# Optimization experiments

Hardware: AMD Instinct MI355X
Metric: run time of the kernel (lower is better)

## Reference

```python
import jax, jax.numpy as jnp
import numpy as np
from jax import lax

T, B = 512, 512
IN_DIM, AUX_DIM, OUT_DIM = 4, 28, 32
G = IN_DIM + AUX_DIM + OUT_DIM  # gate_inputs = 64


def setup_inputs() -> dict:
    key = jax.random.key(0)
    ks = jax.random.split(key, 12)
    s = 0.05
    inp = {
        "xm": jax.random.uniform(ks[0], (T, B, IN_DIM), dtype=jnp.float32),
        "xa": jax.random.normal(ks[1], (T, B, AUX_DIM), dtype=jnp.float32),
        # in_gate (normalized sigmoid): Linear(G -> IN_DIM*OUT_DIM)
        "W_i": jax.random.normal(ks[2], (IN_DIM * OUT_DIM, G), dtype=jnp.float32) * s,
        "b_i": jnp.zeros((IN_DIM * OUT_DIM,), jnp.float32),
        # redistribution (normalized relu): Linear(G -> OUT_DIM*OUT_DIM)
        "W_r": jax.random.normal(ks[3], (OUT_DIM * OUT_DIM, G), dtype=jnp.float32) * s,
        "b_r": jnp.zeros((OUT_DIM * OUT_DIM,), jnp.float32),
        # out_gate: Linear(G -> OUT_DIM), bias init -3.0
        "W_o": jax.random.normal(ks[4], (OUT_DIM, G), dtype=jnp.float32) * s,
        "b_o": jnp.full((OUT_DIM,), -3.0, jnp.float32),
        # MR gate params: weight_s_yvm / weight_r_yvm are (out_features, in_features) = (OUT_DIM, G)
        "W_s": jax.random.normal(ks[5], (OUT_DIM, G), dtype=jnp.float32) * s,
        "W_rm": jax.random.normal(ks[6], (OUT_DIM, G), dtype=jnp.float32) * s,
        "b0": jnp.zeros((OUT_DIM,), jnp.float32),
        "ln_g": jnp.ones((OUT_DIM,), jnp.float32),
        "ln_b": jnp.zeros((OUT_DIM,), jnp.float32),
    }
    return inp


def _l1_normalize(a):
    # torch F.normalize(p=1, dim=-1)
    return a / jnp.maximum(jnp.sum(jnp.abs(a), axis=-1, keepdims=True), 1e-12)


def _layer_norm(x, g, b, eps=1e-5):
    mu = jnp.mean(x, axis=-1, keepdims=True)
    var = jnp.mean((x - mu) ** 2, axis=-1, keepdims=True)
    return (x - mu) * lax.rsqrt(var + eps) * g + b


def reference(xm, xa, W_i, b_i, W_r, b_r, W_o, b_o, W_s, W_rm, b0, ln_g, ln_b):
    Bn = xm.shape[1]
    exp_Ws = jnp.exp(W_s)            # [OUT_DIM, G]
    sig_Wr = jax.nn.sigmoid(W_rm.T)  # [G, OUT_DIM]

    def step(c, ins):
        xm_t, xa_t = ins  # [B, IN_DIM], [B, AUX_DIM]
        # c.norm(1) in torch is the scalar L1 norm over the whole matrix
        c_norm = c / (jnp.sum(jnp.abs(c)) + 1e-5)
        feat = jnp.concatenate([xm_t, xa_t, c_norm], axis=-1)  # [B, G]
        i = _l1_normalize(jax.nn.sigmoid(feat @ W_i.T + b_i).reshape(Bn, IN_DIM, OUT_DIM))
        r = _l1_normalize(jax.nn.relu(feat @ W_r.T + b_r).reshape(Bn, OUT_DIM, OUT_DIM))
        o = jax.nn.sigmoid(feat @ W_o.T + b_o)  # [B, OUT_DIM]
        m_new = jnp.einsum('bi,bio->bo', xm_t, i) + jnp.einsum('bo,bop->bp', c, r)
        # MR gate with f = 1 - o
        f = 1.0 - o
        ov0 = (c_norm - b0) @ exp_Ws          # [B, G]
        ov1 = _layer_norm(jnp.tanh(ov0) @ sig_Wr, ln_g, ln_b)  # [B, OUT_DIM]
        ov2 = ov1 - jax.nn.relu(ov1 - f)
        MR = jax.nn.relu(ov2 + 1.0 - f) + f - 1.0
        o_prime = o + MR
        h = o * m_new
        c_new = (1.0 - o_prime) * m_new
        MR_flow = MR * m_new
        return c_new, (h, c_new, o, MR, o_prime, MR_flow, h)

    c0 = jnp.zeros((Bn, OUT_DIM), xm.dtype)
    _, outs = lax.scan(step, c0, (xm, xa))
    # (hs, cs, os, mrs, o_prime_s, mr_flow_s, o_flow_s), each [T, B, OUT_DIM]
    return outs
```

## Files before the change

### kernel.cpp

```cpp
#include <hip/hip_runtime.h>


#define T_STEPS 512
#define OUTSZ 8388608ull

using bf16v8 = __attribute__((ext_vector_type(8))) short;
using f32v4  = __attribute__((ext_vector_type(4))) float;

__device__ __forceinline__ short f2b(float f) {
  union { float f; unsigned u; } x; x.f = f;
  unsigned r = x.u + 0x7fffu + ((x.u >> 16) & 1u);
  return (short)(r >> 16);
}
__device__ __forceinline__ float rcpf(float x) { return __builtin_amdgcn_rcpf(x); }

__device__ __forceinline__ float rowsum16(float v) {
  int t;
  float a = v;
  t = __builtin_amdgcn_mov_dpp(__builtin_bit_cast(int, a), 0x128, 0xF, 0xF, true);
  a += __builtin_bit_cast(float, t);
  t = __builtin_amdgcn_mov_dpp(__builtin_bit_cast(int, a), 0x124, 0xF, 0xF, true);
  a += __builtin_bit_cast(float, t);
  t = __builtin_amdgcn_mov_dpp(__builtin_bit_cast(int, a), 0x122, 0xF, 0xF, true);
  a += __builtin_bit_cast(float, t);
  t = __builtin_amdgcn_mov_dpp(__builtin_bit_cast(int, a), 0x121, 0xF, 0xF, true);
  a += __builtin_bit_cast(float, t);
  return a;
}

__global__ __launch_bounds__(512, 1) void mclstm_persistent(
    const float* __restrict__ g_xm, const float* __restrict__ g_xa,
    const float* __restrict__ g_Wi, const float* __restrict__ g_bi,
    const float* __restrict__ g_Wr, const float* __restrict__ g_br,
    const float* __restrict__ g_Wo, const float* __restrict__ g_bo,
    const float* __restrict__ g_Ws, const float* __restrict__ g_Wrm,
    const float* __restrict__ g_b0, const float* __restrict__ g_lng,
    const float* __restrict__ g_lnb,
    float* __restrict__ out, float* __restrict__ slots) {

  __shared__ __align__(16) float featx[2][16 * 36];
  __shared__ __align__(16) float cstate[16 * 36];
  __shared__ __align__(16) float gibuf[16 * 132];
  __shared__ __align__(16) float obuf[16 * 36];
  __shared__ __align__(16) float mpart[8][16 * 36];
  __shared__ __align__(16) float isump[128];
  __shared__ __align__(16) unsigned short tanhb[16 * 72];
  __shared__ __align__(16) unsigned short swzSig[4 * 512];
  __shared__ float s_bvec[64], s_lng[32], s_lnb[32];

  const int tid  = threadIdx.x;
  const int blk  = blockIdx.x;
  const int w    = tid >> 6;
  const int lane = tid & 63;
  const int q    = lane >> 4;
  const int m    = lane & 15;
  const f32v4 z4 = {0.f, 0.f, 0.f, 0.f};

  bf16v8 wr0[8], wr1[8];
  float brv[8];
#pragma unroll
  for (int t = 0; t < 8; ++t) {
    const int n = w * 128 + t * 16 + m;
    brv[t] = g_br[n];
#pragma unroll
    for (int kh = 0; kh < 2; ++kh) {
      const float* gp = g_Wr + n * 64 + kh * 32 + q * 8;
      f32v4 u0 = *(const f32v4*)gp;
      f32v4 u1 = *(const f32v4*)(gp + 4);
      bf16v8 fr;
#pragma unroll
      for (int j = 0; j < 4; ++j) { fr[j] = f2b(u0[j]); fr[4 + j] = f2b(u1[j]); }
      if (kh == 0) wr0[t] = fr; else wr1[t] = fr;
    }
  }
  bf16v8 wi0, wi1;
  const float gb = g_bi[w * 16 + m];
  {
    const int n = w * 16 + m;
#pragma unroll
    for (int kh = 0; kh < 2; ++kh) {
      const float* gp = g_Wi + n * 64 + kh * 32 + q * 8;
      f32v4 u0 = *(const f32v4*)gp;
      f32v4 u1 = *(const f32v4*)(gp + 4);
      bf16v8 fr;
#pragma unroll
      for (int j = 0; j < 4; ++j) { fr[j] = f2b(u0[j]); fr[4 + j] = f2b(u1[j]); }
      if (kh == 0) wi0 = fr; else wi1 = fr;
    }
  }
  bf16v8 bo0 = {0,0,0,0,0,0,0,0}, bo1 = bo0, be = bo0;
  float bov = 0.f;
  if (w < 2) {
    const int n = w * 16 + m;
    bov = g_bo[n];
#pragma unroll
    for (int kh = 0; kh < 2; ++kh) {
      bf16v8 fr, fs;
#pragma unroll
      for (int j = 0; j < 8; ++j) {
        fr[j] = f2b(g_Wo[n * 64 + kh * 32 + q * 8 + j]);
        float v = g_Wrm[n * 64 + kh * 32 + q * 8 + j];
        fs[j] = f2b(rcpf(1.0f + __expf(-v)));
      }
      if (kh == 0) bo0 = fr; else bo1 = fr;
      *(bf16v8*)&swzSig[(w * 2 + kh) * 512 + lane * 8] = fs;
    }
  }
  if (w >= 4) {
    const int n = (w - 4) * 16 + m;
    bf16v8 fr;
#pragma unroll
    for (int j = 0; j < 8; ++j) fr[j] = f2b(__expf(g_Ws[(q * 8 + j) * 64 + n]));
    be = fr;
  }
  if (tid < 64) {
    float a = 0.f;
    for (int o = 0; o < 32; ++o) a += g_b0[o] * __expf(g_Ws[o * 64 + tid]);
    s_bvec[tid] = a;
  }
  if (tid < 32) { s_lng[tid] = g_lng[tid]; s_lnb[tid] = g_lnb[tid]; }
  for (int i = tid; i < 16 * 36; i += 512) cstate[i] = 0.0f;
  {
    const int b2 = tid >> 5, k2 = tid & 31, rg = blk * 16 + b2;
    featx[0][b2 * 36 + k2] =
        (k2 < 4) ? g_xm[rg * 4 + k2] : g_xa[rg * 28 + k2 - 4];
  }
  __syncthreads();
  float bvl = (w >= 4) ? s_bvec[(w - 4) * 16 + m] : 0.f;

  float ph_h = 0, ph_cn = 0, ph_o = 0, ph_MR = 0, ph_op = 0, ph_mrf = 0;
  size_t ph_base = 0;

  for (int s = 0; s < T_STEPS; ++s) {
    if (s > 0) {
      out[ph_base] = ph_h;
      out[OUTSZ + ph_base] = ph_cn;
      out[2 * OUTSZ + ph_base] = ph_o;
      out[3 * OUTSZ + ph_base] = ph_MR;
      out[4 * OUTSZ + ph_base] = ph_op;
      out[5 * OUTSZ + ph_base] = ph_mrf;
      out[6 * OUTSZ + ph_base] = ph_h;
    }
    const int b2 = tid >> 5, k2 = tid & 31;
    const int sp = (s + 1 < T_STEPS) ? s + 1 : T_STEPS - 1;
    const float xv = (k2 < 4)
        ? g_xm[(size_t)sp * 2048 + (blk * 16 + b2) * 4 + k2]
        : g_xa[(size_t)sp * 14336 + (blk * 16 + b2) * 28 + k2 - 4];

    const float* fx = featx[s & 1];
    f32v4 x0 = *(const f32v4*)&fx[m * 36 + q * 8];
    f32v4 x1 = *(const f32v4*)&fx[m * 36 + q * 8 + 4];
    f32v4 c0 = *(const f32v4*)&cstate[m * 36 + q * 8];
    f32v4 c1 = *(const f32v4*)&cstate[m * 36 + q * 8 + 4];
    bf16v8 a0, a1;
#pragma unroll
    for (int j = 0; j < 4; ++j) {
      a0[j] = f2b(x0[j]); a0[4 + j] = f2b(x1[j]);
      a1[j] = f2b(c0[j]); a1[4 + j] = f2b(c1[j]);
    }

    f32v4 rx[8], rc[8];
#pragma unroll
    for (int t = 0; t < 8; ++t) {
      f32v4 cb = {brv[t], brv[t], brv[t], brv[t]};
      rx[t] = __builtin_amdgcn_mfma_f32_16x16x32_bf16(a0, wr0[t], cb, 0, 0, 0);
      rc[t] = __builtin_amdgcn_mfma_f32_16x16x32_bf16(a1, wr1[t], z4, 0, 0, 0);
    }
    f32v4 gxb = {gb, gb, gb, gb};
    f32v4 gxv = __builtin_amdgcn_mfma_f32_16x16x32_bf16(a0, wi0, gxb, 0, 0, 0);
    f32v4 gcv = __builtin_amdgcn_mfma_f32_16x16x32_bf16(a1, wi1, z4, 0, 0, 0);
    f32v4 oxv = z4, ocv = z4, ev = z4;
    if (w < 2) {
      f32v4 ob = {bov, bov, bov, bov};
      oxv = __builtin_amdgcn_mfma_f32_16x16x32_bf16(a0, bo0, ob, 0, 0, 0);
      ocv = __builtin_amdgcn_mfma_f32_16x16x32_bf16(a1, bo1, z4, 0, 0, 0);
    }
    if (w >= 4) {
      ev = __builtin_amdgcn_mfma_f32_16x16x32_bf16(a1, be, z4, 0, 0, 0);
    }
    f32v4 c4[4];
#pragma unroll
    for (int r = 0; r < 4; ++r)
      c4[r] = *(const f32v4*)&cstate[(q * 4 + r) * 36 + w * 4];
    featx[(s + 1) & 1][b2 * 36 + k2] = xv;

    float inv_;
    if (s > 0) {
      const float e = ((s >> 1) & 1) ? -1.0f : 1.0f;
      float* sl = slots + (s & 1) * 256 + lane * 4;
      float v0 = 0, v1 = 0, v2 = 0, v3 = 0;
      for (int it = 0; it < (1 << 18); ++it) {
        v0 = __hip_atomic_load(sl + 0, __ATOMIC_RELAXED, __HIP_MEMORY_SCOPE_AGENT);
        v1 = __hip_atomic_load(sl + 1, __ATOMIC_RELAXED, __HIP_MEMORY_SCOPE_AGENT);
        v2 = __hip_atomic_load(sl + 2, __ATOMIC_RELAXED, __HIP_MEMORY_SCOPE_AGENT);
        v3 = __hip_atomic_load(sl + 3, __ATOMIC_RELAXED, __HIP_MEMORY_SCOPE_AGENT);
        if (__all((v0 * e > 0.5f) && (v1 * e > 0.5f) &&
                  (v2 * e > 0.5f) && (v3 * e > 0.5f))) break;
        __builtin_amdgcn_s_sleep(1);
      }
      float sv = rowsum16((v0 + v1 + v2 + v3) * e - 4.0f);
      sv += __shfl_xor(sv, 16);
      sv += __shfl_xor(sv, 32);
      inv_ = rcpf(sv + 1e-5f);
    } else {
      inv_ = rcpf(1e-5f);
    }

    if (w >= 4) {
#pragma unroll
      for (int r = 0; r < 4; ++r) {
        float t0 = ev[r] * inv_ - bvl;
        float ex = __expf(2.0f * t0);
        float th = 1.0f - 2.0f * rcpf(ex + 1.0f);
        tanhb[(q * 4 + r) * 72 + (w - 4) * 16 + m] = (unsigned short)f2b(th);
      }
    }
    if (w < 2) {
#pragma unroll
      for (int r = 0; r < 4; ++r) {
        float t0 = oxv[r] + ocv[r] * inv_;
        obuf[(q * 4 + r) * 36 + w * 16 + m] = rcpf(1.0f + __expf(-t0));
      }
    }
    {
      float sg0, sg1, sg2, sg3;
      {
        float t0 = gxv[0] + gcv[0] * inv_; sg0 = rcpf(1.0f + __expf(-t0));
        t0 = gxv[1] + gcv[1] * inv_; sg1 = rcpf(1.0f + __expf(-t0));
        t0 = gxv[2] + gcv[2] * inv_; sg2 = rcpf(1.0f + __expf(-t0));
        t0 = gxv[3] + gcv[3] * inv_; sg3 = rcpf(1.0f + __expf(-t0));
      }
      gibuf[(q * 4 + 0) * 132 + w * 16 + m] = sg0;
      gibuf[(q * 4 + 1) * 132 + w * 16 + m] = sg1;
      gibuf[(q * 4 + 2) * 132 + w * 16 + m] = sg2;
      gibuf[(q * 4 + 3) * 132 + w * 16 + m] = sg3;
      sg0 = rowsum16(sg0); sg1 = rowsum16(sg1);
      sg2 = rowsum16(sg2); sg3 = rowsum16(sg3);
      if (m == 0) {
        f32v4 sv4 = {sg0, sg1, sg2, sg3};
        *(f32v4*)&isump[w * 16 + q * 4] = sv4;
      }
    }
    {
      f32v4 rr[8];
#pragma unroll
      for (int t = 0; t < 8; ++t)
#pragma unroll
        for (int r = 0; r < 4; ++r)
          rr[t][r] = fmaxf(fmaf(rc[t][r], inv_, rx[t][r]), 0.0f);
      float p0[4] = {0, 0, 0, 0}, p1[4] = {0, 0, 0, 0};
#pragma unroll
      for (int ol = 0; ol < 4; ++ol) {
        float s0 = rowsum16(rr[2 * ol][0] + rr[2 * ol + 1][0]);
        float s1 = rowsum16(rr[2 * ol][1] + rr[2 * ol + 1][1]);
        float s2 = rowsum16(rr[2 * ol][2] + rr[2 * ol + 1][2]);
        float s3 = rowsum16(rr[2 * ol][3] + rr[2 * ol + 1][3]);
        float cr0 = c4[0][ol] * rcpf(fmaxf(s0, 1e-12f));
        float cr1 = c4[1][ol] * rcpf(fmaxf(s1, 1e-12f));
        float cr2 = c4[2][ol] * rcpf(fmaxf(s2, 1e-12f));
        float cr3 = c4[3][ol] * rcpf(fmaxf(s3, 1e-12f));
        p0[0] += rr[2 * ol][0] * cr0; p1[0] += rr[2 * ol + 1][0] * cr0;
        p0[1] += rr[2 * ol][1] * cr1; p1[1] += rr[2 * ol + 1][1] * cr1;
        p0[2] += rr[2 * ol][2] * cr2; p1[2] += rr[2 * ol + 1][2] * cr2;
        p0[3] += rr[2 * ol][3] * cr3; p1[3] += rr[2 * ol + 1][3] * cr3;
      }
#pragma unroll
      for (int r = 0; r < 4; ++r) {
        mpart[w][(q * 4 + r) * 36 + m] = p0[r];
        mpart[w][(q * 4 + r) * 36 + 16 + m] = p1[r];
      }
    }
    __syncthreads();

    {
      bf16v8 a30 = *(const bf16v8*)&tanhb[m * 72 + q * 8];
      bf16v8 a31 = *(const bf16v8*)&tanhb[m * 72 + 32 + q * 8];
      bf16v8 b00 = *(const bf16v8*)&swzSig[0 * 512 + lane * 8];
      bf16v8 b01 = *(const bf16v8*)&swzSig[1 * 512 + lane * 8];
      bf16v8 b10 = *(const bf16v8*)&swzSig[2 * 512 + lane * 8];
      bf16v8 b11 = *(const bf16v8*)&swzSig[3 * 512 + lane * 8];
      f32v4 vA = __builtin_amdgcn_mfma_f32_16x16x32_bf16(a30, b00, z4, 0, 0, 0);
      vA = __builtin_amdgcn_mfma_f32_16x16x32_bf16(a31, b01, vA, 0, 0, 0);
      f32v4 vB = __builtin_amdgcn_mfma_f32_16x16x32_bf16(a30, b10, z4, 0, 0, 0);
      vB = __builtin_amdgcn_mfma_f32_16x16x32_bf16(a31, b11, vB, 0, 0, 0);
      const int b = tid >> 5, p = tid & 31;
      const int srcl = ((b >> 2) << 4) | (p & 15);
      float x00, x01, x10, x11;
      if ((w & 1) == 0) {
        x00 = __shfl(vA[0], srcl); x01 = __shfl(vB[0], srcl);
        x10 = __shfl(vA[1], srcl); x11 = __shfl(vB[1], srcl);
      } else {
        x00 = __shfl(vA[2], srcl); x01 = __shfl(vB[2], srcl);
        x10 = __shfl(vA[3], srcl); x11 = __shfl(vB[3], srcl);
      }
      const bool hiReg = (lane >> 5) != 0;
      const bool hiCol = (p >> 4) != 0;
      float vh0 = hiReg ? x10 : x00;
      float vh1 = hiReg ? x11 : x01;
      float x = hiCol ? vh1 : vh0;

      float s1v = rowsum16(x);      s1v += __shfl_xor(s1v, 16);
      float s2v = rowsum16(x * x);  s2v += __shfl_xor(s2v, 16);
      float mu = s1v * 0.03125f;
      float var = s2v * 0.03125f - mu * mu;
      float ln = (x - mu) * __builtin_amdgcn_rsqf(fmaxf(var, 0.0f) + 1e-5f) *
                     s_lng[p] + s_lnb[p];
      float o = obuf[b * 36 + p];
      float f = 1.0f - o;
      float MR = fmaxf(fminf(ln, f), f - 1.0f);
      float mn = 0.0f;
#pragma unroll
      for (int w2 = 0; w2 < 8; ++w2) mn += mpart[w2][b * 36 + p];
#pragma unroll
      for (int ii = 0; ii < 4; ++ii) {
        float rsi = rcpf(fmaxf(isump[(2 * ii) * 16 + b] +
                               isump[(2 * ii + 1) * 16 + b], 1e-12f));
        mn += fx[b * 36 + ii] * gibuf[b * 132 + ii * 32 + p] * rsi;
      }
      float op = o + MR;
      ph_h = o * mn;
      ph_cn = (1.0f - op) * mn;
      ph_o = o; ph_MR = MR; ph_op = op;
      ph_mrf = MR * mn;
      ph_base = (size_t)s * 16384 + (size_t)(blk * 16 + b) * 32 + p;
      cstate[b * 36 + p] = ph_cn;
      float aw = rowsum16(fabsf(ph_cn));
      aw += __shfl_xor(aw, 16);
      aw += __shfl_xor(aw, 32);
      if (lane == 0 && s + 1 < T_STEPS) {
        const float tag = (((s + 1) >> 1) & 1) ? -1.0f : 1.0f;
        __hip_atomic_store(slots + ((s + 1) & 1) * 256 + blk * 8 + w,
                           tag * (1.0f + aw), __ATOMIC_RELAXED,
                           __HIP_MEMORY_SCOPE_AGENT);
      }
    }
    __syncthreads();
  }
  out[ph_base] = ph_h;
  out[OUTSZ + ph_base] = ph_cn;
  out[2 * OUTSZ + ph_base] = ph_o;
  out[3 * OUTSZ + ph_base] = ph_MR;
  out[4 * OUTSZ + ph_base] = ph_op;
  out[5 * OUTSZ + ph_base] = ph_mrf;
  out[6 * OUTSZ + ph_base] = ph_h;
}

extern "C" void kernel_launch(void* const* d_in, const int* in_sizes, int n_in,
                              void* d_out, int out_size, void* d_ws, size_t ws_size,
                              hipStream_t stream) {
  (void)in_sizes; (void)n_in; (void)out_size; (void)ws_size;
  const float* xm  = (const float*)d_in[0];
  const float* xa  = (const float*)d_in[1];
  const float* Wi  = (const float*)d_in[2];
  const float* bi  = (const float*)d_in[3];
  const float* Wr  = (const float*)d_in[4];
  const float* br  = (const float*)d_in[5];
  const float* Wo  = (const float*)d_in[6];
  const float* bo  = (const float*)d_in[7];
  const float* Ws  = (const float*)d_in[8];
  const float* Wrm = (const float*)d_in[9];
  const float* b0  = (const float*)d_in[10];
  const float* lng = (const float*)d_in[11];
  const float* lnb = (const float*)d_in[12];
  float* slots = (float*)d_ws;

  hipMemsetAsync(d_ws, 0, 2 * 256 * sizeof(float), stream);
  mclstm_persistent<<<dim3(32), dim3(512), 0, stream>>>(
      xm, xa, Wi, bi, Wr, br, Wo, bo, Ws, Wrm, b0, lng, lnb,
      (float*)d_out, slots);
}
```

Before: 2.177 ms.

## Replace per-wave slot flags with a single double atomic-add counter barrier

Each step's cross-block barrier and L1-norm reduction now uses one double-precision atomic add per wave into a single accumulator, with a large offset per arrival acting as a counter. Waiters poll one address until it passes a threshold instead of loading 256 slots and reducing them. Two cross-lane reductions also move to ds_swizzle and readlane in place of shuffles. The atomic-add ordering makes the float sum nondeterministic, and the scheme depends on double precision holding the offset plus the norm, which could cost accuracy. All 256 waves now contend on one address.

```diff
diff --git a/kernel.cpp b/kernel.cpp
--- a/kernel.cpp
+++ b/kernel.cpp
@@ -27,6 +27,14 @@
   a += __builtin_bit_cast(float, t);
   return a;
 }
+__device__ __forceinline__ float xor16f(float x) {
+  int r = __builtin_amdgcn_ds_swizzle(__builtin_bit_cast(int, x), 0x401F);
+  return __builtin_bit_cast(float, r);
+}
+__device__ __forceinline__ float rlanef(float x, int l) {
+  return __builtin_bit_cast(float,
+      __builtin_amdgcn_readlane(__builtin_bit_cast(int, x), l));
+}
 
 __global__ __launch_bounds__(512, 1) void mclstm_persistent(
     const float* __restrict__ g_xm, const float* __restrict__ g_xa,
@@ -55,6 +63,7 @@
   const int q    = lane >> 4;
   const int m    = lane & 15;
   const f32v4 z4 = {0.f, 0.f, 0.f, 0.f};
+  double* slot8 = (double*)slots;
 
   bf16v8 wr0[8], wr1[8];
   float brv[8];
@@ -130,6 +139,7 @@
 
   float ph_h = 0, ph_cn = 0, ph_o = 0, ph_MR = 0, ph_op = 0, ph_mrf = 0;
   size_t ph_base = 0;
+  double base0 = 0.0, base1 = 0.0;
 
   for (int s = 0; s < T_STEPS; ++s) {
     if (s > 0) {
@@ -186,22 +196,19 @@
 
     float inv_;
     if (s > 0) {
-      const float e = ((s >> 1) & 1) ? -1.0f : 1.0f;
-      float* sl = slots + (s & 1) * 256 + lane * 4;
-      float v0 = 0, v1 = 0, v2 = 0, v3 = 0;
-      for (int it = 0; it < (1 << 18); ++it) {
-        v0 = __hip_atomic_load(sl + 0, __ATOMIC_RELAXED, __HIP_MEMORY_SCOPE_AGENT);
-        v1 = __hip_atomic_load(sl + 1, __ATOMIC_RELAXED, __HIP_MEMORY_SCOPE_AGENT);
-        v2 = __hip_atomic_load(sl + 2, __ATOMIC_RELAXED, __HIP_MEMORY_SCOPE_AGENT);
-        v3 = __hip_atomic_load(sl + 3, __ATOMIC_RELAXED, __HIP_MEMORY_SCOPE_AGENT);
-        if (__all((v0 * e > 0.5f) && (v1 * e > 0.5f) &&
-                  (v2 * e > 0.5f) && (v3 * e > 0.5f))) break;
+      const double bse = (s & 1) ? base1 : base0;
+      const double thr = bse + 4286578688.0;
+      const double* sp8 = slot8 + (s & 1);
+      double v  = __hip_atomic_load(sp8, __ATOMIC_RELAXED, __HIP_MEMORY_SCOPE_AGENT);
+      double nx = __hip_atomic_load(sp8, __ATOMIC_RELAXED, __HIP_MEMORY_SCOPE_AGENT);
+      for (int it = 0; (it < (1 << 18)) && (v < thr); ++it) {
+        v = nx;
         __builtin_amdgcn_s_sleep(1);
-      }
-      float sv = rowsum16((v0 + v1 + v2 + v3) * e - 4.0f);
-      sv += __shfl_xor(sv, 16);
-      sv += __shfl_xor(sv, 32);
-      inv_ = rcpf(sv + 1e-5f);
+        nx = __hip_atomic_load(sp8, __ATOMIC_RELAXED, __HIP_MEMORY_SCOPE_AGENT);
+      }
+      if (s & 1) base1 = v; else base0 = v;
+      const float svf = (float)(v - bse - 4294967296.0);
+      inv_ = rcpf(svf + 1e-5f);
     } else {
       inv_ = rcpf(1e-5f);
     }
@@ -299,8 +306,8 @@
       float vh1 = hiReg ? x11 : x01;
       float x = hiCol ? vh1 : vh0;
 
-      float s1v = rowsum16(x);      s1v += __shfl_xor(s1v, 16);
-      float s2v = rowsum16(x * x);  s2v += __shfl_xor(s2v, 16);
+      float s1v = rowsum16(x);      s1v += xor16f(s1v);
+      float s2v = rowsum16(x * x);  s2v += xor16f(s2v);
       float mu = s1v * 0.03125f;
       float var = s2v * 0.03125f - mu * mu;
       float ln = (x - mu) * __builtin_amdgcn_rsqf(fmaxf(var, 0.0f) + 1e-5f) *
@@ -324,14 +331,12 @@
       ph_mrf = MR * mn;
       ph_base = (size_t)s * 16384 + (size_t)(blk * 16 + b) * 32 + p;
       cstate[b * 36 + p] = ph_cn;
-      float aw = rowsum16(fabsf(ph_cn));
-      aw += __shfl_xor(aw, 16);
-      aw += __shfl_xor(aw, 32);
+      float awr = rowsum16(fabsf(ph_cn));
+      float t0 = rlanef(awr, 0),  t1 = rlanef(awr, 16);
+      float t2 = rlanef(awr, 32), t3 = rlanef(awr, 48);
+      float tot = (t0 + t1) + (t2 + t3);
       if (lane == 0 && s + 1 < T_STEPS) {
-        const float tag = (((s + 1) >> 1) & 1) ? -1.0f : 1.0f;
-        __hip_atomic_store(slots + ((s + 1) & 1) * 256 + blk * 8 + w,
-                           tag * (1.0f + aw), __ATOMIC_RELAXED,
-                           __HIP_MEMORY_SCOPE_AGENT);
+        unsafeAtomicAdd(slot8 + ((s + 1) & 1), (double)tot + 16777216.0);
       }
     }
     __syncthreads();
@@ -364,7 +369,7 @@
   const float* lnb = (const float*)d_in[12];
   float* slots = (float*)d_ws;
 
-  hipMemsetAsync(d_ws, 0, 2 * 256 * sizeof(float), stream);
+  hipMemsetAsync(d_ws, 0, 2 * sizeof(double), stream);
   mclstm_persistent<<<dim3(32), dim3(512), 0, stream>>>(
       xm, xa, Wi, bi, Wr, br, Wo, bo, Ws, Wrm, b0, lng, lnb,
       (float*)d_out, slots);
```

New measurement: 3.063 ms. 1.41x slower.

## Split per-block work across 16 waves and use swizzle/readlane reductions

Applied to the files above, without the earlier changes.

Doubles the block size from 512 to 1024 threads, so each wave handles 4 redistribution tiles instead of 8. The in-gate, out-gate and tanh/exp MFMAs move to dedicated wave groups, and the per-step critical path per wave gets shorter. Cross-lane shuffles in the reductions are replaced with ds_swizzle and readlane. The cost is more waves contending at __syncthreads and a larger mpart buffer to sum over 16 partials. The slot-publishing code still assumes 8 writer waves per block and 256 slots.

```diff
diff --git a/kernel.cpp b/kernel.cpp
--- a/kernel.cpp
+++ b/kernel.cpp
@@ -6,6 +6,7 @@
 
 using bf16v8 = __attribute__((ext_vector_type(8))) short;
 using f32v4  = __attribute__((ext_vector_type(4))) float;
+using f32v2  = __attribute__((ext_vector_type(2))) float;
 
 __device__ __forceinline__ short f2b(float f) {
   union { float f; unsigned u; } x; x.f = f;
@@ -27,8 +28,16 @@
   a += __builtin_bit_cast(float, t);
   return a;
 }
-
-__global__ __launch_bounds__(512, 1) void mclstm_persistent(
+__device__ __forceinline__ float xor16f(float x) {
+  int r = __builtin_amdgcn_ds_swizzle(__builtin_bit_cast(int, x), 0x401F);
+  return __builtin_bit_cast(float, r);
+}
+__device__ __forceinline__ float rlanef(float x, int l) {
+  return __builtin_bit_cast(float,
+      __builtin_amdgcn_readlane(__builtin_bit_cast(int, x), l));
+}
+
+__global__ __launch_bounds__(1024, 1) void mclstm_persistent(
     const float* __restrict__ g_xm, const float* __restrict__ g_xa,
     const float* __restrict__ g_Wi, const float* __restrict__ g_bi,
     const float* __restrict__ g_Wr, const float* __restrict__ g_br,
@@ -42,7 +51,7 @@
   __shared__ __align__(16) float cstate[16 * 36];
   __shared__ __align__(16) float gibuf[16 * 132];
   __shared__ __align__(16) float obuf[16 * 36];
-  __shared__ __align__(16) float mpart[8][16 * 36];
+  __shared__ __align__(16) float mpart[16][16 * 36];
   __shared__ __align__(16) float isump[128];
   __shared__ __align__(16) unsigned short tanhb[16 * 72];
   __shared__ __align__(16) unsigned short swzSig[4 * 512];
@@ -56,11 +65,11 @@
   const int m    = lane & 15;
   const f32v4 z4 = {0.f, 0.f, 0.f, 0.f};
 
-  bf16v8 wr0[8], wr1[8];
-  float brv[8];
-#pragma unroll
-  for (int t = 0; t < 8; ++t) {
-    const int n = w * 128 + t * 16 + m;
+  bf16v8 wr0[4], wr1[4];
+  float brv[4];
+#pragma unroll
+  for (int t = 0; t < 4; ++t) {
+    const int n = w * 64 + t * 16 + m;
     brv[t] = g_br[n];
 #pragma unroll
     for (int kh = 0; kh < 2; ++kh) {
@@ -73,10 +82,11 @@
       if (kh == 0) wr0[t] = fr; else wr1[t] = fr;
     }
   }
-  bf16v8 wi0, wi1;
-  const float gb = g_bi[w * 16 + m];
-  {
+  bf16v8 wi0 = {0,0,0,0,0,0,0,0}, wi1 = wi0;
+  float gb = 0.f;
+  if (w < 8) {
     const int n = w * 16 + m;
+    gb = g_bi[n];
 #pragma unroll
     for (int kh = 0; kh < 2; ++kh) {
       const float* gp = g_Wi + n * 64 + kh * 32 + q * 8;
@@ -90,8 +100,8 @@
   }
   bf16v8 bo0 = {0,0,0,0,0,0,0,0}, bo1 = bo0, be = bo0;
   float bov = 0.f;
-  if (w < 2) {
-    const int n = w * 16 + m;
+  if (w == 8 || w == 9) {
+    const int n = (w - 8) * 16 + m;
     bov = g_bo[n];
 #pragma unroll
     for (int kh = 0; kh < 2; ++kh) {
@@ -103,11 +113,11 @@
         fs[j] = f2b(rcpf(1.0f + __expf(-v)));
       }
       if (kh == 0) bo0 = fr; else bo1 = fr;
-      *(bf16v8*)&swzSig[(w * 2 + kh) * 512 + lane * 8] = fs;
-    }
-  }
-  if (w >= 4) {
-    const int n = (w - 4) * 16 + m;
+      *(bf16v8*)&swzSig[((w - 8) * 2 + kh) * 512 + lane * 8] = fs;
+    }
+  }
+  if (w >= 12) {
+    const int n = (w - 12) * 16 + m;
     bf16v8 fr;
 #pragma unroll
     for (int j = 0; j < 8; ++j) fr[j] = f2b(__expf(g_Ws[(q * 8 + j) * 64 + n]));
@@ -119,20 +129,20 @@
     s_bvec[tid] = a;
   }
   if (tid < 32) { s_lng[tid] = g_lng[tid]; s_lnb[tid] = g_lnb[tid]; }
-  for (int i = tid; i < 16 * 36; i += 512) cstate[i] = 0.0f;
-  {
+  for (int i = tid; i < 16 * 36; i += 1024) cstate[i] = 0.0f;
+  if (tid < 512) {
     const int b2 = tid >> 5, k2 = tid & 31, rg = blk * 16 + b2;
     featx[0][b2 * 36 + k2] =
         (k2 < 4) ? g_xm[rg * 4 + k2] : g_xa[rg * 28 + k2 - 4];
   }
   __syncthreads();
-  float bvl = (w >= 4) ? s_bvec[(w - 4) * 16 + m] : 0.f;
+  float bvl = (w >= 12) ? s_bvec[(w - 12) * 16 + m] : 0.f;
 
   float ph_h = 0, ph_cn = 0, ph_o = 0, ph_MR = 0, ph_op = 0, ph_mrf = 0;
   size_t ph_base = 0;
 
   for (int s = 0; s < T_STEPS; ++s) {
-    if (s > 0) {
+    if (s > 0 && w < 8) {
       out[ph_base] = ph_h;
       out[OUTSZ + ph_base] = ph_cn;
       out[2 * OUTSZ + ph_base] = ph_o;
@@ -142,10 +152,13 @@
       out[6 * OUTSZ + ph_base] = ph_h;
     }
     const int b2 = tid >> 5, k2 = tid & 31;
-    const int sp = (s + 1 < T_STEPS) ? s + 1 : T_STEPS - 1;
-    const float xv = (k2 < 4)
-        ? g_xm[(size_t)sp * 2048 + (blk * 16 + b2) * 4 + k2]
-        : g_xa[(size_t)sp * 14336 + (blk * 16 + b2) * 28 + k2 - 4];
+    float xv = 0.f;
+    if (tid < 512) {
+      const int sp = (s + 1 < T_STEPS) ? s + 1 : T_STEPS - 1;
+      xv = (k2 < 4)
+          ? g_xm[(size_t)sp * 2048 + (blk * 16 + b2) * 4 + k2]
+          : g_xa[(size_t)sp * 14336 + (blk * 16 + b2) * 28 + k2 - 4];
+    }
 
     const float* fx = featx[s & 1];
     f32v4 x0 = *(const f32v4*)&fx[m * 36 + q * 8];
@@ -159,30 +172,32 @@
       a1[j] = f2b(c0[j]); a1[4 + j] = f2b(c1[j]);
     }
 
-    f32v4 rx[8], rc[8];
-#pragma unroll
-    for (int t = 0; t < 8; ++t) {
+    f32v4 rx[4], rc[4];
+#pragma unroll
+    for (int t = 0; t < 4; ++t) {
       f32v4 cb = {brv[t], brv[t], brv[t], brv[t]};
       rx[t] = __builtin_amdgcn_mfma_f32_16x16x32_bf16(a0, wr0[t], cb, 0, 0, 0);
       rc[t] = __builtin_amdgcn_mfma_f32_16x16x32_bf16(a1, wr1[t], z4, 0, 0, 0);
     }
-    f32v4 gxb = {gb, gb, gb, gb};
-    f32v4 gxv = __builtin_amdgcn_mfma_f32_16x16x32_bf16(a0, wi0, gxb, 0, 0, 0);
-    f32v4 gcv = __builtin_amdgcn_mfma_f32_16x16x32_bf16(a1, wi1, z4, 0, 0, 0);
-    f32v4 oxv = z4, ocv = z4, ev = z4;
-    if (w < 2) {
+    f32v4 gxv = z4, gcv = z4, oxv = z4, ocv = z4, ev = z4;
+    if (w < 8) {
+      f32v4 gxb = {gb, gb, gb, gb};
+      gxv = __builtin_amdgcn_mfma_f32_16x16x32_bf16(a0, wi0, gxb, 0, 0, 0);
+      gcv = __builtin_amdgcn_mfma_f32_16x16x32_bf16(a1, wi1, z4, 0, 0, 0);
+    }
+    if (w == 8 || w == 9) {
       f32v4 ob = {bov, bov, bov, bov};
       oxv = __builtin_amdgcn_mfma_f32_16x16x32_bf16(a0, bo0, ob, 0, 0, 0);
       ocv = __builtin_amdgcn_mfma_f32_16x16x32_bf16(a1, bo1, z4, 0, 0, 0);
     }
-    if (w >= 4) {
+    if (w >= 12) {
       ev = __builtin_amdgcn_mfma_f32_16x16x32_bf16(a1, be, z4, 0, 0, 0);
     }
-    f32v4 c4[4];
+    f32v2 c2[4];
 #pragma unroll
     for (int r = 0; r < 4; ++r)
-      c4[r] = *(const f32v4*)&cstate[(q * 4 + r) * 36 + w * 4];
-    featx[(s + 1) & 1][b2 * 36 + k2] = xv;
+      c2[r] = *(const f32v2*)&cstate[(q * 4 + r) * 36 + w * 2];
+    if (tid < 512) featx[(s + 1) & 1][b2 * 36 + k2] = xv;
 
     float inv_;
     if (s > 0) {
@@ -199,30 +214,30 @@
         __builtin_amdgcn_s_sleep(1);
       }
       float sv = rowsum16((v0 + v1 + v2 + v3) * e - 4.0f);
-      sv += __shfl_xor(sv, 16);
-      sv += __shfl_xor(sv, 32);
-      inv_ = rcpf(sv + 1e-5f);
+      sv += xor16f(sv);
+      float tot = rlanef(sv, 0) + rlanef(sv, 32);
+      inv_ = rcpf(tot + 1e-5f);
     } else {
       inv_ = rcpf(1e-5f);
     }
 
-    if (w >= 4) {
+    if (w >= 12) {
 #pragma unroll
       for (int r = 0; r < 4; ++r) {
         float t0 = ev[r] * inv_ - bvl;
         float ex = __expf(2.0f * t0);
         float th = 1.0f - 2.0f * rcpf(ex + 1.0f);
-        tanhb[(q * 4 + r) * 72 + (w - 4) * 16 + m] = (unsigned short)f2b(th);
-      }
-    }
-    if (w < 2) {
+        tanhb[(q * 4 + r) * 72 + (w - 12) * 16 + m] = (unsigned short)f2b(th);
+      }
+    }
+    if (w == 8 || w == 9) {
 #pragma unroll
       for (int r = 0; r < 4; ++r) {
         float t0 = oxv[r] + ocv[r] * inv_;
-        obuf[(q * 4 + r) * 36 + w * 16 + m] = rcpf(1.0f + __expf(-t0));
-      }
-    }
-    {
+        obuf[(q * 4 + r) * 36 + (w - 8) * 16 + m] = rcpf(1.0f + __expf(-t0));
+      }
+    }
+    if (w < 8) {
       float sg0, sg1, sg2, sg3;
       {
         float t0 = gxv[0] + gcv[0] * inv_; sg0 = rcpf(1.0f + __expf(-t0));
@@ -242,23 +257,23 @@
       }
     }
     {
-      f32v4 rr[8];
-#pragma unroll
-      for (int t = 0; t < 8; ++t)
+      f32v4 rr[4];
+#pragma unroll
+      for (int t = 0; t < 4; ++t)
 #pragma unroll
         for (int r = 0; r < 4; ++r)
           rr[t][r] = fmaxf(fmaf(rc[t][r], inv_, rx[t][r]), 0.0f);
       float p0[4] = {0, 0, 0, 0}, p1[4] = {0, 0, 0, 0};
 #pragma unroll
-      for (int ol = 0; ol < 4; ++ol) {
+      for (int ol = 0; ol < 2; ++ol) {
         float s0 = rowsum16(rr[2 * ol][0] + rr[2 * ol + 1][0]);
         float s1 = rowsum16(rr[2 * ol][1] + rr[2 * ol + 1][1]);
         float s2 = rowsum16(rr[2 * ol][2] + rr[2 * ol + 1][2]);
         float s3 = rowsum16(rr[2 * ol][3] + rr[2 * ol + 1][3]);
-        float cr0 = c4[0][ol] * rcpf(fmaxf(s0, 1e-12f));
-        float cr1 = c4[1][ol] * rcpf(fmaxf(s1, 1e-12f));
-        float cr2 = c4[2][ol] * rcpf(fmaxf(s2, 1e-12f));
-        float cr3 = c4[3][ol] * rcpf(fmaxf(s3, 1e-12f));
+        float cr0 = c2[0][ol] * rcpf(fmaxf(s0, 1e-12f));
+        float cr1 = c2[1][ol] * rcpf(fmaxf(s1, 1e-12f));
+        float cr2 = c2[2][ol] * rcpf(fmaxf(s2, 1e-12f));
+        float cr3 = c2[3][ol] * rcpf(fmaxf(s3, 1e-12f));
         p0[0] += rr[2 * ol][0] * cr0; p1[0] += rr[2 * ol + 1][0] * cr0;
         p0[1] += rr[2 * ol][1] * cr1; p1[1] += rr[2 * ol + 1][1] * cr1;
         p0[2] += rr[2 * ol][2] * cr2; p1[2] += rr[2 * ol + 1][2] * cr2;
@@ -272,7 +287,7 @@
     }
     __syncthreads();
 
-    {
+    if (w < 8) {
       bf16v8 a30 = *(const bf16v8*)&tanhb[m * 72 + q * 8];
       bf16v8 a31 = *(const bf16v8*)&tanhb[m * 72 + 32 + q * 8];
       bf16v8 b00 = *(const bf16v8*)&swzSig[0 * 512 + lane * 8];
@@ -299,8 +314,8 @@
       float vh1 = hiReg ? x11 : x01;
       float x = hiCol ? vh1 : vh0;
 
-      float s1v = rowsum16(x);      s1v += __shfl_xor(s1v, 16);
-      float s2v = rowsum16(x * x);  s2v += __shfl_xor(s2v, 16);
+      float s1v = rowsum16(x);      s1v += xor16f(s1v);
+      float s2v = rowsum16(x * x);  s2v += xor16f(s2v);
       float mu = s1v * 0.03125f;
       float var = s2v * 0.03125f - mu * mu;
       float ln = (x - mu) * __builtin_amdgcn_rsqf(fmaxf(var, 0.0f) + 1e-5f) *
@@ -310,7 +325,7 @@
       float MR = fmaxf(fminf(ln, f), f - 1.0f);
       float mn = 0.0f;
 #pragma unroll
-      for (int w2 = 0; w2 < 8; ++w2) mn += mpart[w2][b * 36 + p];
+      for (int w2 = 0; w2 < 16; ++w2) mn += mpart[w2][b * 36 + p];
 #pragma unroll
       for (int ii = 0; ii < 4; ++ii) {
         float rsi = rcpf(fmaxf(isump[(2 * ii) * 16 + b] +
@@ -324,25 +339,27 @@
       ph_mrf = MR * mn;
       ph_base = (size_t)s * 16384 + (size_t)(blk * 16 + b) * 32 + p;
       cstate[b * 36 + p] = ph_cn;
-      float aw = rowsum16(fabsf(ph_cn));
-      aw += __shfl_xor(aw, 16);
-      aw += __shfl_xor(aw, 32);
+      float awr = rowsum16(fabsf(ph_cn));
+      awr += xor16f(awr);
+      float tot = rlanef(awr, 0) + rlanef(awr, 32);
       if (lane == 0 && s + 1 < T_STEPS) {
         const float tag = (((s + 1) >> 1) & 1) ? -1.0f : 1.0f;
         __hip_atomic_store(slots + ((s + 1) & 1) * 256 + blk * 8 + w,
-                           tag * (1.0f + aw), __ATOMIC_RELAXED,
+                           tag * (1.0f + tot), __ATOMIC_RELAXED,
                            __HIP_MEMORY_SCOPE_AGENT);
       }
     }
     __syncthreads();
   }
-  out[ph_base] = ph_h;
-  out[OUTSZ + ph_base] = ph_cn;
-  out[2 * OUTSZ + ph_base] = ph_o;
-  out[3 * OUTSZ + ph_base] = ph_MR;
-  out[4 * OUTSZ + ph_base] = ph_op;
-  out[5 * OUTSZ + ph_base] = ph_mrf;
-  out[6 * OUTSZ + ph_base] = ph_h;
+  if (w < 8) {
+    out[ph_base] = ph_h;
+    out[OUTSZ + ph_base] = ph_cn;
+    out[2 * OUTSZ + ph_base] = ph_o;
+    out[3 * OUTSZ + ph_base] = ph_MR;
+    out[4 * OUTSZ + ph_base] = ph_op;
+    out[5 * OUTSZ + ph_base] = ph_mrf;
+    out[6 * OUTSZ + ph_base] = ph_h;
+  }
 }
 
 extern "C" void kernel_launch(void* const* d_in, const int* in_sizes, int n_in,
@@ -365,7 +382,7 @@
   float* slots = (float*)d_ws;
 
   hipMemsetAsync(d_ws, 0, 2 * 256 * sizeof(float), stream);
-  mclstm_persistent<<<dim3(32), dim3(512), 0, stream>>>(
+  mclstm_persistent<<<dim3(32), dim3(1024), 0, stream>>>(
       xm, xa, Wi, bi, Wr, br, Wo, bo, Ws, Wrm, b0, lng, lnb,
       (float*)d_out, slots);
 }
```

Result: slower. 4.195 ms (+92.7%).
